# Kernel optimization log

Hardware: AMD Instinct MI355X
Metric: run time of the kernel (lower is better)

The kernel has to match this reference:

```python
import jax, jax.numpy as jnp
import numpy as np

B, T, E, H, M2 = 8, 2048, 256, 2, 134
HD = E // H


def setup_inputs() -> dict:
    key = jax.random.key(0)
    ks = jax.random.split(key, 10)
    s = 0.02
    return {
        "X": jax.random.normal(ks[0], (B, T, E), dtype=jnp.float32),
        "Y": jax.random.uniform(ks[1], (B, M2), dtype=jnp.float32),
        "wpe": s * jax.random.normal(ks[2], (T, E), dtype=jnp.float32),
        "ln1_g": jnp.ones((E,), jnp.float32), "ln1_b": jnp.zeros((E,), jnp.float32),
        "attn_w": s * jax.random.normal(ks[3], (3 * E, E), dtype=jnp.float32),
        "attn_b": jnp.zeros((3 * E,), jnp.float32),
        "attnproj_w": s * jax.random.normal(ks[4], (E, E), dtype=jnp.float32),
        "attnproj_b": jnp.zeros((E,), jnp.float32),
        "ln2_g": jnp.ones((E,), jnp.float32), "ln2_b": jnp.zeros((E,), jnp.float32),
        "fc_w": s * jax.random.normal(ks[5], (2 * E, E), dtype=jnp.float32),
        "fc_b": jnp.zeros((2 * E,), jnp.float32),
        "mlpproj_w": s * jax.random.normal(ks[6], (E, 2 * E), dtype=jnp.float32),
        "mlpproj_b": jnp.zeros((E,), jnp.float32),
        "lnf_g": jnp.ones((E,), jnp.float32), "lnf_b": jnp.zeros((E,), jnp.float32),
        "head_w": s * jax.random.normal(ks[7], (M2, E), dtype=jnp.float32),
        "head_b": jnp.zeros((M2,), jnp.float32),
    }


def _ln(x, g, b, eps=1e-5):
    mu = x.mean(-1, keepdims=True)
    var = ((x - mu) ** 2).mean(-1, keepdims=True)
    return (x - mu) * jax.lax.rsqrt(var + eps) * g + b


def reference(X, Y, wpe, ln1_g, ln1_b, attn_w, attn_b, attnproj_w, attnproj_b,
              ln2_g, ln2_b, fc_w, fc_b, mlpproj_w, mlpproj_b, lnf_g, lnf_b,
              head_w, head_b):
    # positional ids = arange(T) -> wpe itself; cls ids = [0]*T/2 + [1]*T/2
    cls_ids = np.concatenate([np.zeros(T // 2, np.int32), np.ones(T // 2, np.int32)])
    x = X + wpe + wpe[cls_ids]                      # [B,T,E] (dropout = identity, eval)

    # single Block (n_layer=1), preceded by ReLU as in cross_mod loop
    x = jax.nn.relu(x)
    h = _ln(x, ln1_g, ln1_b)
    qkv = h @ attn_w.T + attn_b                     # [B,T,3E]
    q, k, v = jnp.split(qkv, 3, axis=-1)
    q, k, v = jax.nn.relu(q), jax.nn.relu(k), jax.nn.relu(v)
    split_heads = lambda t: t.reshape(B, T, H, HD).transpose(0, 2, 1, 3)
    q, k, v = split_heads(q), split_heads(k), split_heads(v)
    att = jnp.einsum('bhqd,bhkd->bhqk', q, k) * (1.0 / np.sqrt(HD))
    tril = jnp.tril(jnp.ones((T, T), dtype=bool))
    # masked_fill(-inf) then ReLU  ==  zero outside causal mask, ReLU inside
    att = jnp.where(tril, jax.nn.relu(att), 0.0)    # [B,H,T,T]
    y = jnp.einsum('bhqk,bhkd->bhqd', att, v)
    y = y.transpose(0, 2, 1, 3).reshape(B, T, E)
    x = x + (y @ attnproj_w.T + attnproj_b)

    h = _ln(x, ln2_g, ln2_b)
    x = x + (jax.nn.relu(h @ fc_w.T + fc_b) @ mlpproj_w.T + mlpproj_b)

    x = jax.nn.relu(x)
    x = _ln(x, lnf_g, lnf_b)
    x = jax.nn.relu(x)
    emb = x.mean(axis=1)                            # [B,E]
    logits = jax.nn.relu(emb @ head_w.T + head_b)   # [B,M2]

    loss1 = jnp.sqrt(jnp.mean((logits - Y) ** 2))
    e1, e2 = emb[:, : E // 2], emb[:, E // 2:]
    loss3 = jnp.sqrt(jnp.mean((e1 - e2) ** 2))
    loss = 50.0 * loss1 + loss3
    return (e1, e2, loss, loss1, loss3, logits)
```

## Files before the change

kernel.cpp:

```cpp
#include <hip/hip_runtime.h>
#include <hip/hip_bf16.h>

#define Bc 8
#define Tc 2048
#define Ec 256
#define Hc 2
#define HDc 128
#define Mrows (Bc*Tc)
#define M2c 134

using bfx8  = __attribute__((ext_vector_type(8))) __bf16;
using bfx4  = __attribute__((ext_vector_type(4))) __bf16;
using f32x4 = __attribute__((ext_vector_type(4))) float;

__device__ __forceinline__ void gll16(const __bf16* g, __bf16* lds) {
    __builtin_amdgcn_global_load_lds(
        (const __attribute__((address_space(1))) unsigned int*)g,
        (__attribute__((address_space(3))) unsigned int*)lds, 16, 0, 0);
}

__global__ __launch_bounds__(256) void embed_prep_k(const float* X, const float* wpe,
                                                    const float* g, const float* bb,
                                                    const float* attn_w, const float* apw,
                                                    const float* fcw, const float* mpw,
                                                    __bf16* wb, float* embsum,
                                                    __bf16* xres, __bf16* hb) {
    int tid = threadIdx.x, w = tid >> 6, l = tid & 63;
    int bidx = blockIdx.x;
    if (bidx < 2048) {
        int i = bidx * 256 + tid;
        if (i < 196608)       wb[i] = (__bf16)attn_w[i];
        else if (i < 262144)  wb[i] = (__bf16)apw[i - 196608];
        else if (i < 393216)  wb[i] = (__bf16)fcw[i - 262144];
        else                  wb[i] = (__bf16)mpw[i - 393216];
        if (bidx < 8) embsum[bidx * 256 + tid] = 0.f;
    }
    int m = bidx * 4 + w;
    int t = m & (Tc - 1);
    int e0 = l * 4;
    float4 x  = *(const float4*)(X   + (size_t)m * Ec + e0);
    float4 p1 = *(const float4*)(wpe + (size_t)t * Ec + e0);
    float4 p2 = *(const float4*)(wpe + (size_t)(t >= 1024 ? Ec : 0) + e0);
    float v0 = fmaxf(x.x + p1.x + p2.x, 0.f);
    float v1 = fmaxf(x.y + p1.y + p2.y, 0.f);
    float v2 = fmaxf(x.z + p1.z + p2.z, 0.f);
    float v3 = fmaxf(x.w + p1.w + p2.w, 0.f);
    bfx4 xq; xq[0] = (__bf16)v0; xq[1] = (__bf16)v1; xq[2] = (__bf16)v2; xq[3] = (__bf16)v3;
    *(bfx4*)(xres + (size_t)m * Ec + e0) = xq;
    float s1 = v0 + v1 + v2 + v3;
    float s2 = v0 * v0 + v1 * v1 + v2 * v2 + v3 * v3;
    #pragma unroll
    for (int o = 32; o; o >>= 1) { s1 += __shfl_xor(s1, o, 64); s2 += __shfl_xor(s2, o, 64); }
    float m1 = s1 * (1.f / 256.f), m2 = s2 * (1.f / 256.f);
    float r = rsqrtf(m2 - m1 * m1 + 1e-5f);
    float4 gg = *(const float4*)(g + e0);
    float4 bv = *(const float4*)(bb + e0);
    bfx4 hq;
    hq[0] = (__bf16)((v0 - m1) * r * gg.x + bv.x);
    hq[1] = (__bf16)((v1 - m1) * r * gg.y + bv.y);
    hq[2] = (__bf16)((v2 - m1) * r * gg.z + bv.z);
    hq[3] = (__bf16)((v3 - m1) * r * gg.w + bv.w);
    *(bfx4*)(hb + (size_t)m * Ec + e0) = hq;
}

__global__ __launch_bounds__(256) void gemm_qkv(const __bf16* __restrict__ A,
                                                const __bf16* __restrict__ Bw,
                                                const float* __restrict__ bias,
                                                __bf16* __restrict__ Qb,
                                                __bf16* __restrict__ Kb,
                                                __bf16* __restrict__ Vt) {
    const int K = 256;
    __shared__ __attribute__((aligned(16))) __bf16 smem[128 * 136];
    __bf16* As = smem;
    __bf16* Bs = smem + 128 * 64;
    const int tid = threadIdx.x, w = tid >> 6, l = tid & 63;
    const int m0 = blockIdx.y * 128, n0 = blockIdx.x * 128;
    const int wr = w >> 1, wc = w & 1;
    const int quad = l >> 4, col15 = l & 15;

    f32x4 acc[4][4];
    f32x4 zz = {0.f, 0.f, 0.f, 0.f};
    #pragma unroll
    for (int i = 0; i < 4; i++)
        #pragma unroll
        for (int j = 0; j < 4; j++) acc[i][j] = zz;

    const int lrow = l >> 3;
    const int pbs  = l & 7;

    for (int kb = 0; kb < K; kb += 64) {
        #pragma unroll
        for (int it = 0; it < 4; it++) {
            int chunk = w * 4 + it;
            int row = chunk * 8 + lrow;
            int lb = pbs ^ (row & 7);
            gll16(A  + (size_t)(m0 + row) * K + kb + lb * 8, As + chunk * 512);
            gll16(Bw + (size_t)(n0 + row) * K + kb + lb * 8, Bs + chunk * 512);
        }
        __syncthreads();
        #pragma unroll
        for (int ks = 0; ks < 2; ks++) {
            bfx8 af[4], bfr[4];
            #pragma unroll
            for (int rt = 0; rt < 4; rt++) {
                int row = wr * 64 + rt * 16 + col15;
                int pb = (ks * 4 + quad) ^ (row & 7);
                af[rt] = *(const bfx8*)(As + row * 64 + pb * 8);
            }
            #pragma unroll
            for (int ct = 0; ct < 4; ct++) {
                int row = wc * 64 + ct * 16 + col15;
                int pb = (ks * 4 + quad) ^ (row & 7);
                bfr[ct] = *(const bfx8*)(Bs + row * 64 + pb * 8);
            }
            #pragma unroll
            for (int rt = 0; rt < 4; rt++)
                #pragma unroll
                for (int ct = 0; ct < 4; ct++)
                    acc[rt][ct] = __builtin_amdgcn_mfma_f32_16x16x32_bf16(af[rt], bfr[ct], acc[rt][ct], 0, 0, 0);
        }
        __syncthreads();
    }

    if (n0 < 512) {
        #pragma unroll
        for (int rt = 0; rt < 4; rt++)
            #pragma unroll
            for (int ct = 0; ct < 4; ct++) {
                int mgb = m0 + wr * 64 + rt * 16 + quad * 4;
                int ng  = n0 + wc * 64 + ct * 16 + col15;
                float bsv = bias[ng];
                #pragma unroll
                for (int r = 0; r < 4; r++) {
                    float val = fmaxf(acc[rt][ct][r] + bsv, 0.f);
                    int mg = mgb + r;
                    int sel = ng >> 8;
                    int hh = (ng >> 7) & 1;
                    int d = ng & 127;
                    int bb2 = mg >> 11, tt = mg & (Tc - 1);
                    size_t idx = ((size_t)((bb2 * 2 + hh) * Tc + tt)) * HDc + d;
                    __bf16 bv = (__bf16)val;
                    if (sel == 0) Qb[idx] = bv;
                    else Kb[idx] = bv;
                }
            }
    } else {
        int hh = (n0 >> 7) & 1;
        int bh = (m0 >> 11) * 2 + hh;
        #pragma unroll
        for (int rt = 0; rt < 4; rt++)
            #pragma unroll
            for (int ct = 0; ct < 4; ct++) {
                int d  = wc * 64 + ct * 16 + col15;
                float bsv = bias[n0 + wc * 64 + ct * 16 + col15];
                #pragma unroll
                for (int r = 0; r < 4; r++) {
                    int tt = wr * 64 + rt * 16 + quad * 4 + r;
                    float val = fmaxf(acc[rt][ct][r] + bsv, 0.f);
                    smem[d * 136 + tt] = (__bf16)val;
                }
            }
        __syncthreads();
        #pragma unroll
        for (int it = 0; it < 8; it++) {
            int d  = w * 32 + it * 4 + (l >> 4);
            int t0 = (l & 15) * 8;
            bfx8 vv = *(const bfx8*)(smem + d * 136 + t0);
            *(bfx8*)(Vt + ((size_t)(bh * HDc + d)) * Tc + m0 + t0) = vv;
        }
    }
}

__global__ __launch_bounds__(512, 4) void attn6_k(const __bf16* __restrict__ Qb,
                                                  const __bf16* __restrict__ Kb,
                                                  const __bf16* __restrict__ Vt,
                                                  __bf16* __restrict__ Y1,
                                                  __bf16* __restrict__ Y2,
                                                  __bf16* __restrict__ Y3,
                                                  __bf16* __restrict__ Y4) {
    __shared__ __bf16 Ks[2][64 * 128];
    __shared__ __bf16 Vs[2][64 * 128];
    __shared__ __bf16 Ss[128 * 64];
    int bid = blockIdx.x;
    int lane8 = bid & 7;
    int s = bid >> 3;
    int bh = ((s & 1) << 3) | lane8;
    int f = s >> 1;
    int qt, ch;
    if (f < 16)      { qt = 12 + (f >> 2);          ch = f & 3; }
    else if (f < 28) { int r = f - 16; int d3 = r / 3; qt = 8 + d3; ch = r - 3 * d3; }
    else if (f < 36) { qt = 4 + ((f - 28) >> 1);    ch = (f - 28) & 1; }
    else             { qt = f - 36;                 ch = 0; }
    int Q0 = qt * 128;
    int kts = ch * 8;
    int kte = min(kts + 8, 2 * qt + 2);

    int tid = threadIdx.x, w = tid >> 6, l = tid & 63;
    int quad = l >> 4, col15 = l & 15;
    const int qs = w >> 1, kh = w & 1;
    const int lrowK = l >> 4, pbsK = l & 15;
    const int lrowV = l >> 3, pbsV = l & 7;

    __bf16* Qs = &Ks[0][0];
    #pragma unroll
    for (int it = 0; it < 4; it++) {
        int chunk = w * 4 + it;
        int row = chunk * 4 + lrowK;
        int lb = pbsK ^ (row & 7);
        gll16(Qb + ((size_t)(bh * Tc + Q0 + row)) * HDc + lb * 8, Qs + chunk * 512);
    }
    __syncthreads();
    bfx8 qf[2][4];
    #pragma unroll
    for (int rt = 0; rt < 2; rt++)
        #pragma unroll
        for (int ks = 0; ks < 4; ks++) {
            int row = qs * 32 + rt * 16 + col15;
            int pb = (ks * 4 + quad) ^ (row & 7);
            qf[rt][ks] = *(const bfx8*)(Qs + row * 128 + pb * 8);
        }
    __syncthreads();

    f32x4 zz = {0.f, 0.f, 0.f, 0.f};
    f32x4 yacc[2][4];
    #pragma unroll
    for (int rt = 0; rt < 2; rt++)
        #pragma unroll
        for (int dt = 0; dt < 4; dt++) yacc[rt][dt] = zz;

    auto stageKV = [&](int buf, int kt) {
        #pragma unroll
        for (int it = 0; it < 2; it++) {
            int chunk = w * 2 + it;
            int rowK = chunk * 4 + lrowK;
            int lbK = pbsK ^ (rowK & 7);
            gll16(Kb + ((size_t)(bh * Tc + kt * 64 + rowK)) * HDc + lbK * 8, Ks[buf] + chunk * 512);
            int rowV = chunk * 8 + lrowV;
            int lbV = pbsV ^ (rowV & 7);
            gll16(Vt + ((size_t)(bh * HDc + rowV)) * Tc + kt * 64 + lbV * 8, Vs[buf] + chunk * 512);
        }
    };

    stageKV(0, kts);
    int cur = 0;
    for (int kt = kts; kt < kte; kt++) {
        __syncthreads();
        if (kt + 1 < kte) stageKV(cur ^ 1, kt + 1);

        f32x4 sacc[2][2];
        #pragma unroll
        for (int rt = 0; rt < 2; rt++)
            #pragma unroll
            for (int ct = 0; ct < 2; ct++) sacc[rt][ct] = zz;
        #pragma unroll
        for (int ks = 0; ks < 4; ks++) {
            #pragma unroll
            for (int ct = 0; ct < 2; ct++) {
                int row = kh * 32 + ct * 16 + col15;
                int pb = (ks * 4 + quad) ^ (row & 7);
                bfx8 kf = *(const bfx8*)(Ks[cur] + row * 128 + pb * 8);
                #pragma unroll
                for (int rt = 0; rt < 2; rt++)
                    sacc[rt][ct] = __builtin_amdgcn_mfma_f32_16x16x32_bf16(qf[rt][ks], kf, sacc[rt][ct], 0, 0, 0);
            }
        }

        #pragma unroll
        for (int ct = 0; ct < 2; ct++) {
            int kl = kh * 32 + ct * 16 + col15;
            int kg = kt * 64 + kl;
            int blk = kl >> 3, off = kl & 7;
            #pragma unroll
            for (int rt = 0; rt < 2; rt++)
                #pragma unroll
                for (int r = 0; r < 4; r++) {
                    int qlw = qs * 32 + rt * 16 + quad * 4 + r;
                    float val = (kg <= Q0 + qlw) ? fmaxf(sacc[rt][ct][r], 0.f) : 0.f;
                    int pb = blk ^ (qlw & 7);
                    Ss[qlw * 64 + pb * 8 + off] = (__bf16)val;
                }
        }

        asm volatile("s_waitcnt lgkmcnt(0)" ::: "memory");
        __builtin_amdgcn_s_barrier();
        __builtin_amdgcn_sched_barrier(0);

        #pragma unroll
        for (int ks = 0; ks < 2; ks++) {
            bfx8 sf[2];
            #pragma unroll
            for (int rt = 0; rt < 2; rt++) {
                int rowS = qs * 32 + rt * 16 + col15;
                int pbS = (ks * 4 + quad) ^ (rowS & 7);
                sf[rt] = *(const bfx8*)(Ss + rowS * 64 + pbS * 8);
            }
            #pragma unroll
            for (int dt = 0; dt < 4; dt++) {
                int rowV = kh * 64 + dt * 16 + col15;
                int pb = (ks * 4 + quad) ^ (rowV & 7);
                bfx8 vf = *(const bfx8*)(Vs[cur] + rowV * 64 + pb * 8);
                #pragma unroll
                for (int rt = 0; rt < 2; rt++)
                    yacc[rt][dt] = __builtin_amdgcn_mfma_f32_16x16x32_bf16(sf[rt], vf, yacc[rt][dt], 0, 0, 0);
            }
        }
        cur ^= 1;
    }

    __bf16* Yp = (ch == 0) ? Y1 : (ch == 1) ? Y2 : (ch == 2) ? Y3 : Y4;
    int b = bh >> 1, h = bh & 1;
    const float sc = 0.08838834764831845f;
    #pragma unroll
    for (int rt = 0; rt < 2; rt++)
        #pragma unroll
        for (int dt = 0; dt < 4; dt++) {
            int d = kh * 64 + dt * 16 + col15;
            #pragma unroll
            for (int r = 0; r < 4; r++) {
                int q = Q0 + qs * 32 + rt * 16 + quad * 4 + r;
                Yp[((size_t)(b * Tc + q)) * Ec + h * HDc + d] = (__bf16)(yacc[rt][dt][r] * sc);
            }
        }
}

__global__ __launch_bounds__(512, 1) void mega_k(const __bf16* __restrict__ Y1,
                                                 const __bf16* __restrict__ Y2,
                                                 const __bf16* __restrict__ Y3,
                                                 const __bf16* __restrict__ Y4,
                                                 const __bf16* __restrict__ wap,
                                                 const float* __restrict__ apb,
                                                 const __bf16* __restrict__ xres,
                                                 const float* __restrict__ ln2_g,
                                                 const float* __restrict__ ln2_b,
                                                 const __bf16* __restrict__ wfc,
                                                 const float* __restrict__ fcb,
                                                 const __bf16* __restrict__ wmp,
                                                 const float* __restrict__ mpb,
                                                 const float* __restrict__ lnf_g,
                                                 const float* __restrict__ lnf_b,
                                                 float* __restrict__ embsum) {
    __shared__ __bf16 h2s[4 * 4096];
    __shared__ __bf16 fc64[8 * 4096];
    __shared__ __bf16 Bs[256 * 64];
    __shared__ float ps1[64][8], ps2[64][8];
    __shared__ float mus[64], rss[64];
    const int tid = threadIdx.x, w = tid >> 6, l = tid & 63;
    const int m0 = blockIdx.x * 64;
    const int quad = l >> 4, col15 = l & 15;
    const int lrow = l >> 3, pbs = l & 7;
    const int n0 = w * 32;
    f32x4 zz = {0.f, 0.f, 0.f, 0.f};

    const int nsum = (((m0 & (Tc - 1)) >> 6) + 8) >> 3;
    __bf16* As = fc64;

    const int arow_s = tid >> 3;
    const int ablk   = tid & 7;

    auto loadY = [&](int kb) -> bfx8 {
        size_t off = (size_t)(m0 + arow_s) * 256 + kb + ablk * 8;
        bfx8 a1 = *(const bfx8*)(Y1 + off);
        float tmp[8];
        #pragma unroll
        for (int jj = 0; jj < 8; jj++) tmp[jj] = (float)a1[jj];
        if (nsum > 1) { bfx8 aj = *(const bfx8*)(Y2 + off);
            #pragma unroll
            for (int jj = 0; jj < 8; jj++) tmp[jj] += (float)aj[jj]; }
        if (nsum > 2) { bfx8 aj = *(const bfx8*)(Y3 + off);
            #pragma unroll
            for (int jj = 0; jj < 8; jj++) tmp[jj] += (float)aj[jj]; }
        if (nsum > 3) { bfx8 aj = *(const bfx8*)(Y4 + off);
            #pragma unroll
            for (int jj = 0; jj < 8; jj++) tmp[jj] += (float)aj[jj]; }
        #pragma unroll
        for (int jj = 0; jj < 8; jj++) a1[jj] = (__bf16)tmp[jj];
        return a1;
    };

    f32x4 acc[4][2];
    #pragma unroll
    for (int rt = 0; rt < 4; rt++)
        #pragma unroll
        for (int ct = 0; ct < 2; ct++) acc[rt][ct] = zz;

    bfx8 av = loadY(0);

    for (int kb = 0; kb < 256; kb += 64) {
        __syncthreads();
        { int pb = ablk ^ (arow_s & 7);
          *(bfx8*)(As + arow_s * 64 + pb * 8) = av; }
        #pragma unroll
        for (int it = 0; it < 4; it++) {
            int chunk = w * 4 + it;
            int row = chunk * 8 + lrow;
            int lb = pbs ^ (row & 7);
            gll16(wap + (size_t)row * 256 + kb + lb * 8, Bs + chunk * 512);
        }
        bfx8 avn;
        if (kb < 192) avn = loadY(kb + 64);
        __syncthreads();
        #pragma unroll
        for (int ks = 0; ks < 2; ks++) {
            bfx8 af[4];
            #pragma unroll
            for (int rt = 0; rt < 4; rt++) {
                int ar = rt * 16 + col15;
                int apbk = (ks * 4 + quad) ^ (ar & 7);
                af[rt] = *(const bfx8*)(As + ar * 64 + apbk * 8);
            }
            #pragma unroll
            for (int ct = 0; ct < 2; ct++) {
                int br = n0 + ct * 16 + col15;
                int bpb = (ks * 4 + quad) ^ (br & 7);
                bfx8 bf = *(const bfx8*)(Bs + br * 64 + bpb * 8);
                #pragma unroll
                for (int rt = 0; rt < 4; rt++)
                    acc[rt][ct] = __builtin_amdgcn_mfma_f32_16x16x32_bf16(af[rt], bf, acc[rt][ct], 0, 0, 0);
            }
        }
        if (kb < 192) av = avn;
    }

    float xv[4][2][4];
    #pragma unroll
    for (int ct = 0; ct < 2; ct++) {
        int ng = n0 + ct * 16 + col15;
        float bsv = apb[ng];
        #pragma unroll
        for (int rt = 0; rt < 4; rt++)
            #pragma unroll
            for (int r = 0; r < 4; r++) {
                int mg = m0 + rt * 16 + quad * 4 + r;
                xv[rt][ct][r] = acc[rt][ct][r] + bsv + (float)xres[(size_t)mg * 256 + ng];
            }
    }
    #pragma unroll
    for (int rt = 0; rt < 4; rt++)
        #pragma unroll
        for (int r = 0; r < 4; r++) {
            float a  = xv[rt][0][r] + xv[rt][1][r];
            float b2 = xv[rt][0][r] * xv[rt][0][r] + xv[rt][1][r] * xv[rt][1][r];
            #pragma unroll
            for (int o = 1; o < 16; o <<= 1) { a += __shfl_xor(a, o, 64); b2 += __shfl_xor(b2, o, 64); }
            if (col15 == 0) { int row = rt * 16 + quad * 4 + r; ps1[row][w] = a; ps2[row][w] = b2; }
        }
    __syncthreads();
    {
        int row = tid >> 3, widx = tid & 7;
        float a = ps1[row][widx], b2 = ps2[row][widx];
        #pragma unroll
        for (int o = 1; o < 8; o <<= 1) { a += __shfl_xor(a, o, 64); b2 += __shfl_xor(b2, o, 64); }
        if ((l & 7) == 0) {
            float mu = a * (1.f / 256.f);
            float var = b2 * (1.f / 256.f) - mu * mu;
            mus[row] = mu; rss[row] = rsqrtf(var + 1e-5f);
        }
    }
    __syncthreads();
    #pragma unroll
    for (int ct = 0; ct < 2; ct++) {
        int ng = n0 + ct * 16 + col15;
        float gv = ln2_g[ng], bv = ln2_b[ng];
        int panel = ng >> 6, c = ng & 63;
        #pragma unroll
        for (int rt = 0; rt < 4; rt++)
            #pragma unroll
            for (int r = 0; r < 4; r++) {
                int row = rt * 16 + quad * 4 + r;
                float h = (xv[rt][ct][r] - mus[row]) * rss[row] * gv + bv;
                h2s[panel * 4096 + row * 64 + ((c >> 3) ^ (row & 7)) * 8 + (c & 7)] = (__bf16)h;
            }
    }

    for (int half = 0; half < 2; half++) {
        f32x4 acc2[4][2];
        #pragma unroll
        for (int rt = 0; rt < 4; rt++)
            #pragma unroll
            for (int ct = 0; ct < 2; ct++) acc2[rt][ct] = zz;
        for (int kb = 0; kb < 256; kb += 64) {
            __syncthreads();
            #pragma unroll
            for (int it = 0; it < 4; it++) {
                int chunk = w * 4 + it;
                int row = chunk * 8 + lrow;
                int lb = pbs ^ (row & 7);
                gll16(wfc + (size_t)(half * 256 + row) * 256 + kb + lb * 8, Bs + chunk * 512);
            }
            __syncthreads();
            int panel = kb >> 6;
            #pragma unroll
            for (int ks = 0; ks < 2; ks++) {
                bfx8 af[4];
                #pragma unroll
                for (int rt = 0; rt < 4; rt++) {
                    int ar = rt * 16 + col15;
                    int apbk = (ks * 4 + quad) ^ (ar & 7);
                    af[rt] = *(const bfx8*)(h2s + panel * 4096 + ar * 64 + apbk * 8);
                }
                #pragma unroll
                for (int ct = 0; ct < 2; ct++) {
                    int br = n0 + ct * 16 + col15;
                    int bpb = (ks * 4 + quad) ^ (br & 7);
                    bfx8 bf = *(const bfx8*)(Bs + br * 64 + bpb * 8);
                    #pragma unroll
                    for (int rt = 0; rt < 4; rt++)
                        acc2[rt][ct] = __builtin_amdgcn_mfma_f32_16x16x32_bf16(af[rt], bf, acc2[rt][ct], 0, 0, 0);
                }
            }
        }
        #pragma unroll
        for (int ct = 0; ct < 2; ct++) {
            int col = half * 256 + n0 + ct * 16 + col15;
            float bsv = fcb[col];
            int panel = col >> 6, c = col & 63;
            #pragma unroll
            for (int rt = 0; rt < 4; rt++)
                #pragma unroll
                for (int r = 0; r < 4; r++) {
                    int row = rt * 16 + quad * 4 + r;
                    float val = fmaxf(acc2[rt][ct][r] + bsv, 0.f);
                    fc64[panel * 4096 + row * 64 + ((c >> 3) ^ (row & 7)) * 8 + (c & 7)] = (__bf16)val;
                }
        }
    }

    #pragma unroll
    for (int rt = 0; rt < 4; rt++)
        #pragma unroll
        for (int ct = 0; ct < 2; ct++) acc[rt][ct] = zz;
    for (int kb = 0; kb < 512; kb += 64) {
        __syncthreads();
        #pragma unroll
        for (int it = 0; it < 4; it++) {
            int chunk = w * 4 + it;
            int row = chunk * 8 + lrow;
            int lb = pbs ^ (row & 7);
            gll16(wmp + (size_t)row * 512 + kb + lb * 8, Bs + chunk * 512);
        }
        __syncthreads();
        int panel = kb >> 6;
        #pragma unroll
        for (int ks = 0; ks < 2; ks++) {
            bfx8 af[4];
            #pragma unroll
            for (int rt = 0; rt < 4; rt++) {
                int ar = rt * 16 + col15;
                int apbk = (ks * 4 + quad) ^ (ar & 7);
                af[rt] = *(const bfx8*)(fc64 + panel * 4096 + ar * 64 + apbk * 8);
            }
            #pragma unroll
            for (int ct = 0; ct < 2; ct++) {
                int br = n0 + ct * 16 + col15;
                int bpb = (ks * 4 + quad) ^ (br & 7);
                bfx8 bf = *(const bfx8*)(Bs + br * 64 + bpb * 8);
                #pragma unroll
                for (int rt = 0; rt < 4; rt++)
                    acc[rt][ct] = __builtin_amdgcn_mfma_f32_16x16x32_bf16(af[rt], bf, acc[rt][ct], 0, 0, 0);
            }
        }
    }

    #pragma unroll
    for (int ct = 0; ct < 2; ct++) {
        int ng = n0 + ct * 16 + col15;
        float bsv = mpb[ng];
        #pragma unroll
        for (int rt = 0; rt < 4; rt++)
            #pragma unroll
            for (int r = 0; r < 4; r++)
                xv[rt][ct][r] = fmaxf(acc[rt][ct][r] + bsv + xv[rt][ct][r], 0.f);
    }
    #pragma unroll
    for (int rt = 0; rt < 4; rt++)
        #pragma unroll
        for (int r = 0; r < 4; r++) {
            float a  = xv[rt][0][r] + xv[rt][1][r];
            float b2 = xv[rt][0][r] * xv[rt][0][r] + xv[rt][1][r] * xv[rt][1][r];
            #pragma unroll
            for (int o = 1; o < 16; o <<= 1) { a += __shfl_xor(a, o, 64); b2 += __shfl_xor(b2, o, 64); }
            if (col15 == 0) { int row = rt * 16 + quad * 4 + r; ps1[row][w] = a; ps2[row][w] = b2; }
        }
    __syncthreads();
    {
        int row = tid >> 3, widx = tid & 7;
        float a = ps1[row][widx], b2 = ps2[row][widx];
        #pragma unroll
        for (int o = 1; o < 8; o <<= 1) { a += __shfl_xor(a, o, 64); b2 += __shfl_xor(b2, o, 64); }
        if ((l & 7) == 0) {
            float mu = a * (1.f / 256.f);
            float var = b2 * (1.f / 256.f) - mu * mu;
            mus[row] = mu; rss[row] = rsqrtf(var + 1e-5f);
        }
    }
    __syncthreads();
    #pragma unroll
    for (int ct = 0; ct < 2; ct++) {
        int ng = n0 + ct * 16 + col15;
        float gv = lnf_g[ng], bv = lnf_b[ng];
        float csum = 0.f;
        #pragma unroll
        for (int rt = 0; rt < 4; rt++)
            #pragma unroll
            for (int r = 0; r < 4; r++) {
                int row = rt * 16 + quad * 4 + r;
                float h = (xv[rt][ct][r] - mus[row]) * rss[row] * gv + bv;
                csum += fmaxf(h, 0.f);
            }
        csum += __shfl_xor(csum, 16, 64);
        csum += __shfl_xor(csum, 32, 64);
        if (quad == 0) atomicAdd(&embsum[(m0 >> 11) * 256 + ng], csum);
    }
}

__global__ __launch_bounds__(256) void final_k(const float* embsum, const float* Yt,
                                               const float* head_w, const float* head_b,
                                               float* out) {
    __shared__ float semb[2048];
    __shared__ float slog[1072];
    int tid = threadIdx.x;
    for (int i = tid; i < 2048; i += 256) semb[i] = embsum[i] * (1.f / 2048.f);
    __syncthreads();
    float part1 = 0.f;
    for (int idx = tid; idx < 1072; idx += 256) {
        int b = idx / M2c, n = idx - b * M2c;
        float acc = head_b[n];
        const float* wn = head_w + (size_t)n * Ec;
        const float* e = semb + b * Ec;
        #pragma unroll 8
        for (int k = 0; k < Ec; k++) acc += e[k] * wn[k];
        acc = fmaxf(acc, 0.f);
        slog[idx] = acc;
        float d = acc - Yt[idx];
        part1 += d * d;
    }
    float part3 = 0.f;
    for (int idx = tid; idx < 1024; idx += 256) {
        int b = idx >> 7, i = idx & 127;
        float d = semb[b * Ec + i] - semb[b * Ec + 128 + i];
        part3 += d * d;
    }
    #pragma unroll
    for (int o = 32; o; o >>= 1) { part1 += __shfl_xor(part1, o, 64); part3 += __shfl_xor(part3, o, 64); }
    __shared__ float r1[4], r3[4];
    int w = tid >> 6;
    if ((tid & 63) == 0) { r1[w] = part1; r3[w] = part3; }
    __syncthreads();
    float l1 = sqrtf((r1[0] + r1[1] + r1[2] + r1[3]) / 1072.f);
    float l3 = sqrtf((r3[0] + r3[1] + r3[2] + r3[3]) / 1024.f);
    for (int idx = tid; idx < 1024; idx += 256) {
        int b = idx >> 7, i = idx & 127;
        out[idx]        = semb[b * Ec + i];
        out[1024 + idx] = semb[b * Ec + 128 + i];
    }
    if (tid == 0) {
        out[2048] = 50.f * l1 + l3;
        out[2049] = l1;
        out[2050] = l3;
    }
    for (int idx = tid; idx < 1072; idx += 256) out[2051 + idx] = slog[idx];
}

extern "C" void kernel_launch(void* const* d_in, const int* in_sizes, int n_in,
                              void* d_out, int out_size, void* d_ws, size_t ws_size,
                              hipStream_t stream) {
    const float* X        = (const float*)d_in[0];
    const float* Yt       = (const float*)d_in[1];
    const float* wpe      = (const float*)d_in[2];
    const float* ln1_g    = (const float*)d_in[3];
    const float* ln1_b    = (const float*)d_in[4];
    const float* attn_w   = (const float*)d_in[5];
    const float* attn_b   = (const float*)d_in[6];
    const float* apw      = (const float*)d_in[7];
    const float* apb      = (const float*)d_in[8];
    const float* ln2_g    = (const float*)d_in[9];
    const float* ln2_b    = (const float*)d_in[10];
    const float* fcw      = (const float*)d_in[11];
    const float* fcb      = (const float*)d_in[12];
    const float* mpw      = (const float*)d_in[13];
    const float* mpb      = (const float*)d_in[14];
    const float* lnf_g    = (const float*)d_in[15];
    const float* lnf_b    = (const float*)d_in[16];
    const float* head_w   = (const float*)d_in[17];
    const float* head_b   = (const float*)d_in[18];

    char* ws = (char*)d_ws;
    const size_t MB = 1048576;
    __bf16* xres   = (__bf16*)(ws + 0 * MB);
    __bf16* hb     = (__bf16*)(ws + 8 * MB);
    __bf16* Qb     = (__bf16*)(ws + 16 * MB);
    __bf16* Kb     = (__bf16*)(ws + 24 * MB);
    __bf16* Vb     = (__bf16*)(ws + 32 * MB);
    __bf16* Vt     = (__bf16*)(ws + 40 * MB);
    __bf16* Y1     = (__bf16*)(ws + 48 * MB);
    __bf16* Y2     = (__bf16*)(ws + 56 * MB);
    __bf16* wb     = (__bf16*)(ws + 64 * MB);
    float*  embsum = (float*)(ws + 65 * MB);

    __bf16* Y3 = hb;
    __bf16* Y4 = Vb;

    __bf16* wqkv = wb;
    __bf16* wap  = wb + 196608;
    __bf16* wfc  = wb + 262144;
    __bf16* wmp  = wb + 393216;

    embed_prep_k<<<4096, 256, 0, stream>>>(X, wpe, ln1_g, ln1_b,
                                           attn_w, apw, fcw, mpw, wb, embsum, xres, hb);
    gemm_qkv<<<dim3(6, 128), 256, 0, stream>>>(hb, wqkv, attn_b, Qb, Kb, Vt);
    attn6_k<<<640, 512, 0, stream>>>(Qb, Kb, Vt, Y1, Y2, Y3, Y4);
    mega_k<<<256, 512, 0, stream>>>(Y1, Y2, Y3, Y4, wap, apb, xres, ln2_g, ln2_b,
                                    wfc, fcb, wmp, mpb, lnf_g, lnf_b, embsum);
    final_k<<<1, 256, 0, stream>>>(embsum, Yt, head_w, head_b, (float*)d_out);
}
```

Baseline: 223.1 us.

## Pack attention score stores and load MLP weights straight to registers

The attention score MFMA now takes its operands in swapped order, so each lane holds four consecutive key positions and writes them to LDS as one packed bfx4 store instead of four scalar stores. In mega_k, the weight tiles for the attn-proj, fc and mlp-proj GEMMs are read from global memory directly into registers with double buffering. This drops the shared Bs staging buffer and the two barriers per k-step. It also fixes the V-transpose store offset to use the in-sequence time index rather than the global row index. In exchange, register pressure goes up and there are more uncoalesced global weight loads per wave, which now depend on L2 hits.

```diff
diff --git a/kernel.cpp b/kernel.cpp
--- a/kernel.cpp
+++ b/kernel.cpp
@@ -147,6 +147,7 @@
     } else {
         int hh = (n0 >> 7) & 1;
         int bh = (m0 >> 11) * 2 + hh;
+        int tbase = m0 & (Tc - 1);
         #pragma unroll
         for (int rt = 0; rt < 4; rt++)
             #pragma unroll
@@ -166,7 +167,7 @@
             int d  = w * 32 + it * 4 + (l >> 4);
             int t0 = (l & 15) * 8;
             bfx8 vv = *(const bfx8*)(smem + d * 136 + t0);
-            *(bfx8*)(Vt + ((size_t)(bh * HDc + d)) * Tc + m0 + t0) = vv;
+            *(bfx8*)(Vt + ((size_t)(bh * HDc + d)) * Tc + tbase + t0) = vv;
         }
     }
 }
@@ -249,9 +250,9 @@
 
         f32x4 sacc[2][2];
         #pragma unroll
-        for (int rt = 0; rt < 2; rt++)
-            #pragma unroll
-            for (int ct = 0; ct < 2; ct++) sacc[rt][ct] = zz;
+        for (int ct = 0; ct < 2; ct++)
+            #pragma unroll
+            for (int rt = 0; rt < 2; rt++) sacc[ct][rt] = zz;
         #pragma unroll
         for (int ks = 0; ks < 4; ks++) {
             #pragma unroll
@@ -261,24 +262,27 @@
                 bfx8 kf = *(const bfx8*)(Ks[cur] + row * 128 + pb * 8);
                 #pragma unroll
                 for (int rt = 0; rt < 2; rt++)
-                    sacc[rt][ct] = __builtin_amdgcn_mfma_f32_16x16x32_bf16(qf[rt][ks], kf, sacc[rt][ct], 0, 0, 0);
+                    sacc[ct][rt] = __builtin_amdgcn_mfma_f32_16x16x32_bf16(kf, qf[rt][ks], sacc[ct][rt], 0, 0, 0);
             }
         }
 
         #pragma unroll
         for (int ct = 0; ct < 2; ct++) {
-            int kl = kh * 32 + ct * 16 + col15;
-            int kg = kt * 64 + kl;
-            int blk = kl >> 3, off = kl & 7;
-            #pragma unroll
-            for (int rt = 0; rt < 2; rt++)
+            int kbase = kh * 32 + ct * 16 + quad * 4;
+            int kgb = kt * 64 + kbase;
+            #pragma unroll
+            for (int rt = 0; rt < 2; rt++) {
+                int qlocal = qs * 32 + rt * 16 + col15;
+                int qg = Q0 + qlocal;
+                bfx4 pack;
                 #pragma unroll
                 for (int r = 0; r < 4; r++) {
-                    int qlw = qs * 32 + rt * 16 + quad * 4 + r;
-                    float val = (kg <= Q0 + qlw) ? fmaxf(sacc[rt][ct][r], 0.f) : 0.f;
-                    int pb = blk ^ (qlw & 7);
-                    Ss[qlw * 64 + pb * 8 + off] = (__bf16)val;
+                    float val = (kgb + r <= qg) ? fmaxf(sacc[ct][rt][r], 0.f) : 0.f;
+                    pack[r] = (__bf16)val;
                 }
+                int pb = (kbase >> 3) ^ (qlocal & 7);
+                *(bfx4*)(Ss + qlocal * 64 + pb * 8 + (kbase & 7)) = pack;
+            }
         }
 
         asm volatile("s_waitcnt lgkmcnt(0)" ::: "memory");
@@ -341,13 +345,11 @@
                                                  float* __restrict__ embsum) {
     __shared__ __bf16 h2s[4 * 4096];
     __shared__ __bf16 fc64[8 * 4096];
-    __shared__ __bf16 Bs[256 * 64];
     __shared__ float ps1[64][8], ps2[64][8];
     __shared__ float mus[64], rss[64];
     const int tid = threadIdx.x, w = tid >> 6, l = tid & 63;
     const int m0 = blockIdx.x * 64;
     const int quad = l >> 4, col15 = l & 15;
-    const int lrow = l >> 3, pbs = l & 7;
     const int n0 = w * 32;
     f32x4 zz = {0.f, 0.f, 0.f, 0.f};
 
@@ -377,6 +379,16 @@
         return a1;
     };
 
+    auto loadB = [&](const __bf16* W, int stride, int kb, bfx8 (&out)[2][2]) {
+        #pragma unroll
+        for (int ks = 0; ks < 2; ks++)
+            #pragma unroll
+            for (int ct = 0; ct < 2; ct++) {
+                int br = n0 + ct * 16 + col15;
+                out[ks][ct] = *(const bfx8*)(W + (size_t)br * stride + kb + (ks * 4 + quad) * 8);
+            }
+    };
+
     f32x4 acc[4][2];
     #pragma unroll
     for (int rt = 0; rt < 4; rt++)
@@ -384,20 +396,15 @@
         for (int ct = 0; ct < 2; ct++) acc[rt][ct] = zz;
 
     bfx8 av = loadY(0);
+    bfx8 bw[2][2];
+    loadB(wap, 256, 0, bw);
 
     for (int kb = 0; kb < 256; kb += 64) {
         __syncthreads();
         { int pb = ablk ^ (arow_s & 7);
           *(bfx8*)(As + arow_s * 64 + pb * 8) = av; }
-        #pragma unroll
-        for (int it = 0; it < 4; it++) {
-            int chunk = w * 4 + it;
-            int row = chunk * 8 + lrow;
-            int lb = pbs ^ (row & 7);
-            gll16(wap + (size_t)row * 256 + kb + lb * 8, Bs + chunk * 512);
-        }
-        bfx8 avn;
-        if (kb < 192) avn = loadY(kb + 64);
+        bfx8 avn; bfx8 bwn[2][2];
+        if (kb < 192) { avn = loadY(kb + 64); loadB(wap, 256, kb + 64, bwn); }
         __syncthreads();
         #pragma unroll
         for (int ks = 0; ks < 2; ks++) {
@@ -409,16 +416,18 @@
                 af[rt] = *(const bfx8*)(As + ar * 64 + apbk * 8);
             }
             #pragma unroll
-            for (int ct = 0; ct < 2; ct++) {
-                int br = n0 + ct * 16 + col15;
-                int bpb = (ks * 4 + quad) ^ (br & 7);
-                bfx8 bf = *(const bfx8*)(Bs + br * 64 + bpb * 8);
+            for (int ct = 0; ct < 2; ct++)
                 #pragma unroll
                 for (int rt = 0; rt < 4; rt++)
-                    acc[rt][ct] = __builtin_amdgcn_mfma_f32_16x16x32_bf16(af[rt], bf, acc[rt][ct], 0, 0, 0);
-            }
-        }
-        if (kb < 192) av = avn;
+                    acc[rt][ct] = __builtin_amdgcn_mfma_f32_16x16x32_bf16(af[rt], bw[ks][ct], acc[rt][ct], 0, 0, 0);
+        }
+        if (kb < 192) {
+            av = avn;
+            #pragma unroll
+            for (int ks = 0; ks < 2; ks++)
+                #pragma unroll
+                for (int ct = 0; ct < 2; ct++) bw[ks][ct] = bwn[ks][ct];
+        }
     }
 
     float xv[4][2][4];
@@ -471,24 +480,22 @@
                 h2s[panel * 4096 + row * 64 + ((c >> 3) ^ (row & 7)) * 8 + (c & 7)] = (__bf16)h;
             }
     }
-
+    __syncthreads();
+
+    #pragma unroll
     for (int half = 0; half < 2; half++) {
+        const __bf16* Wh = wfc + (size_t)(half * 256) * 256;
         f32x4 acc2[4][2];
         #pragma unroll
         for (int rt = 0; rt < 4; rt++)
             #pragma unroll
             for (int ct = 0; ct < 2; ct++) acc2[rt][ct] = zz;
-        for (int kb = 0; kb < 256; kb += 64) {
-            __syncthreads();
-            #pragma unroll
-            for (int it = 0; it < 4; it++) {
-                int chunk = w * 4 + it;
-                int row = chunk * 8 + lrow;
-                int lb = pbs ^ (row & 7);
-                gll16(wfc + (size_t)(half * 256 + row) * 256 + kb + lb * 8, Bs + chunk * 512);
-            }
-            __syncthreads();
-            int panel = kb >> 6;
+        bfx8 breg[2][2][2];
+        loadB(Wh, 256, 0, breg[0]);
+        #pragma unroll
+        for (int kb6 = 0; kb6 < 4; kb6++) {
+            int cur = kb6 & 1;
+            if (kb6 < 3) loadB(Wh, 256, (kb6 + 1) * 64, breg[cur ^ 1]);
             #pragma unroll
             for (int ks = 0; ks < 2; ks++) {
                 bfx8 af[4];
@@ -496,17 +503,13 @@
                 for (int rt = 0; rt < 4; rt++) {
                     int ar = rt * 16 + col15;
                     int apbk = (ks * 4 + quad) ^ (ar & 7);
-                    af[rt] = *(const bfx8*)(h2s + panel * 4096 + ar * 64 + apbk * 8);
+                    af[rt] = *(const bfx8*)(h2s + kb6 * 4096 + ar * 64 + apbk * 8);
                 }
                 #pragma unroll
-                for (int ct = 0; ct < 2; ct++) {
-                    int br = n0 + ct * 16 + col15;
-                    int bpb = (ks * 4 + quad) ^ (br & 7);
-                    bfx8 bf = *(const bfx8*)(Bs + br * 64 + bpb * 8);
+                for (int ct = 0; ct < 2; ct++)
                     #pragma unroll
                     for (int rt = 0; rt < 4; rt++)
-                        acc2[rt][ct] = __builtin_amdgcn_mfma_f32_16x16x32_bf16(af[rt], bf, acc2[rt][ct], 0, 0, 0);
-                }
+                        acc2[rt][ct] = __builtin_amdgcn_mfma_f32_16x16x32_bf16(af[rt], breg[cur][ks][ct], acc2[rt][ct], 0, 0, 0);
             }
         }
         #pragma unroll
@@ -524,39 +527,33 @@
                 }
         }
     }
+    __syncthreads();
 
     #pragma unroll
     for (int rt = 0; rt < 4; rt++)
         #pragma unroll
         for (int ct = 0; ct < 2; ct++) acc[rt][ct] = zz;
-    for (int kb = 0; kb < 512; kb += 64) {
-        __syncthreads();
-        #pragma unroll
-        for (int it = 0; it < 4; it++) {
-            int chunk = w * 4 + it;
-            int row = chunk * 8 + lrow;
-            int lb = pbs ^ (row & 7);
-            gll16(wmp + (size_t)row * 512 + kb + lb * 8, Bs + chunk * 512);
-        }
-        __syncthreads();
-        int panel = kb >> 6;
-        #pragma unroll
-        for (int ks = 0; ks < 2; ks++) {
-            bfx8 af[4];
-            #pragma unroll
-            for (int rt = 0; rt < 4; rt++) {
-                int ar = rt * 16 + col15;
-                int apbk = (ks * 4 + quad) ^ (ar & 7);
-                af[rt] = *(const bfx8*)(fc64 + panel * 4096 + ar * 64 + apbk * 8);
-            }
-            #pragma unroll
-            for (int ct = 0; ct < 2; ct++) {
-                int br = n0 + ct * 16 + col15;
-                int bpb = (ks * 4 + quad) ^ (br & 7);
-                bfx8 bf = *(const bfx8*)(Bs + br * 64 + bpb * 8);
-                #pragma unroll
-                for (int rt = 0; rt < 4; rt++)
-                    acc[rt][ct] = __builtin_amdgcn_mfma_f32_16x16x32_bf16(af[rt], bf, acc[rt][ct], 0, 0, 0);
+    {
+        bfx8 breg[2][2][2];
+        loadB(wmp, 512, 0, breg[0]);
+        #pragma unroll
+        for (int kb6 = 0; kb6 < 8; kb6++) {
+            int cur = kb6 & 1;
+            if (kb6 < 7) loadB(wmp, 512, (kb6 + 1) * 64, breg[cur ^ 1]);
+            #pragma unroll
+            for (int ks = 0; ks < 2; ks++) {
+                bfx8 af[4];
+                #pragma unroll
+                for (int rt = 0; rt < 4; rt++) {
+                    int ar = rt * 16 + col15;
+                    int apbk = (ks * 4 + quad) ^ (ar & 7);
+                    af[rt] = *(const bfx8*)(fc64 + kb6 * 4096 + ar * 64 + apbk * 8);
+                }
+                #pragma unroll
+                for (int ct = 0; ct < 2; ct++)
+                    #pragma unroll
+                    for (int rt = 0; rt < 4; rt++)
+                        acc[rt][ct] = __builtin_amdgcn_mfma_f32_16x16x32_bf16(af[rt], breg[cur][ks][ct], acc[rt][ct], 0, 0, 0);
             }
         }
     }
```

New measurement: 224.3 us. Within noise of the previous version (+0.6%).
